# Performance work log

Hardware: AMD Instinct MI355X
Metric: run time of the kernel (lower is better)

The kernel has to match this reference:

```python
import jax, jax.numpy as jnp
import numpy as np

NODE_DIM = 128
CTX_DIM = 256
OUT_DIM = 256
GRID_SIZE = 4
SPLINE_ORDER = 3
IN_DIM = 3 * NODE_DIM  # subj + obj + transformed context
N_NODES = 100000
N_EDGES = 100000


def make_grid(in_dim, grid_size, spline_order, grid_range=(-1.0, 1.0)):
    h = (grid_range[1] - grid_range[0]) / grid_size
    g = (np.arange(-spline_order, grid_size + spline_order + 1, dtype=np.float32) * h
         + grid_range[0])  # [grid_size + 2*spline_order + 1]
    return jnp.asarray(np.tile(g[None, :], (in_dim, 1)))  # [in, G]


def b_splines(x, grid, spline_order):
    # x: [N, in], grid: [in, G] -> bases: [N, in, grid_size + spline_order]
    xg = x[:, :, None]
    bases = ((xg >= grid[:, :-1]) & (xg < grid[:, 1:])).astype(x.dtype)
    for k in range(1, spline_order + 1):
        left = (xg - grid[:, : -(k + 1)]) / (grid[:, k:-1] - grid[:, : -(k + 1)]) * bases[..., :-1]
        right = (grid[:, k + 1:] - xg) / (grid[:, k + 1:] - grid[:, 1:-k]) * bases[..., 1:]
        bases = left + right
    return bases


def setup_inputs() -> dict:
    key = jax.random.key(0)
    ks = jax.random.split(key, 8)
    n_coef = GRID_SIZE + SPLINE_ORDER
    return {
        "node_embeddings": jax.random.normal(ks[0], (N_NODES, NODE_DIM), jnp.float32),
        "context_embeddings": jax.random.normal(ks[1], (N_EDGES, CTX_DIM), jnp.float32),
        "pair_indices": jax.random.randint(ks[2], (N_EDGES, 2), 0, N_NODES, jnp.int64 if jax.config.jax_enable_x64 else jnp.int32),
        "ctx_w": jax.random.normal(ks[3], (NODE_DIM, CTX_DIM), jnp.float32) * (1.0 / np.sqrt(CTX_DIM)),
        "ctx_b": jnp.zeros((NODE_DIM,), jnp.float32),
        "base_weight": jax.random.normal(ks[4], (OUT_DIM, IN_DIM), jnp.float32) * (1.0 / np.sqrt(IN_DIM)),
        "spline_weight": jax.random.normal(ks[5], (OUT_DIM, IN_DIM, n_coef), jnp.float32) * 0.1,
        "spline_scaler": jax.random.normal(ks[6], (OUT_DIM, IN_DIM), jnp.float32) * (1.0 / np.sqrt(IN_DIM)),
        "grid": make_grid(IN_DIM, GRID_SIZE, SPLINE_ORDER),
    }


def reference(node_embeddings, context_embeddings, pair_indices, ctx_w, ctx_b,
              base_weight, spline_weight, spline_scaler, grid):
    # gather subject/object node embeddings (irregular access)
    subj = node_embeddings[pair_indices[:, 0]]          # [E, node_dim]
    obj = node_embeddings[pair_indices[:, 1]]           # [E, node_dim]
    ctx = context_embeddings @ ctx_w.T + ctx_b          # [E, node_dim]
    x = jnp.concatenate([subj, obj, ctx], axis=1)       # [E, 3*node_dim]

    # efficient-KAN linear layer: base (SiLU) branch + B-spline branch
    base_out = jax.nn.silu(x) @ base_weight.T           # [E, out]
    bsp = b_splines(x, grid, SPLINE_ORDER)              # [E, in, n_coef]
    scaled_w = spline_weight * spline_scaler[:, :, None]  # [out, in, n_coef]
    spline_out = jnp.einsum('nic,oic->no', bsp, scaled_w)
    return base_out + spline_out
```

## Files before the change

kernel.cpp:

```cpp
#include <hip/hip_runtime.h>

#define NEDGES   100000
#define NODE_DIM 128
#define CTX_DIM  256
#define OUT_DIM  256
#define IN_DIM   384
#define NCOEF    7

#define BM2      128
#define BK2      32
#define NCH2     96
#define THR2     512

typedef __bf16 bf16x8 __attribute__((ext_vector_type(8)));
typedef float  f32x4  __attribute__((ext_vector_type(4)));

static __device__ __forceinline__ unsigned short f2bf(float f) {
    unsigned int u = __float_as_uint(f);
    u += 0x7FFFu + ((u >> 16) & 1u);
    return (unsigned short)(u >> 16);
}
static __device__ __forceinline__ float bf2f(unsigned short h) {
    return __uint_as_float(((unsigned int)h) << 16);
}
static __device__ __forceinline__ unsigned int pkbf(float a, float b) {
    unsigned int ua = __float_as_uint(a), ub = __float_as_uint(b);
    ua += 0x7FFFu + ((ua >> 16) & 1u);
    ub += 0x7FFFu + ((ub >> 16) & 1u);
    return (ua >> 16) | (ub & 0xFFFF0000u);
}
static __device__ __forceinline__ float silu(float x) {
    return x / (1.0f + __expf(-x));
}
static __device__ __forceinline__ float n3(float t) {
    float d2 = t - 2.0f;
    float a  = fabsf(d2);
    float p1 = fmaf(fmaf(0.5f, a, -1.0f), d2 * d2, 0.66666667f);
    float dd = fmaxf(2.0f - a, 0.0f);
    float p2 = dd * dd * (dd * (1.0f / 6.0f));
    return a < 1.0f ? p1 : p2;
}

static __device__ __forceinline__ void glds16(const unsigned short* g, unsigned short* l) {
    __builtin_amdgcn_global_load_lds(
        (const __attribute__((address_space(1))) void*)g,
        (__attribute__((address_space(3))) void*)l, 16, 0, 0);
}

__global__ void prep_w2(const float* __restrict__ base_w,
                        const float* __restrict__ spline_w,
                        const float* __restrict__ spline_s,
                        unsigned short* __restrict__ Wsw)
{
    int o = blockIdx.x;
    int i = threadIdx.x;
    int bi = o * IN_DIM + i;
    float sc = spline_s[bi];
    const float* sw = spline_w + (size_t)bi * NCOEF;
    uint4 v;
    v.x = pkbf(base_w[bi], sw[0] * sc);
    v.y = pkbf(sw[1] * sc, sw[2] * sc);
    v.z = pkbf(sw[3] * sc, sw[4] * sc);
    v.w = pkbf(sw[5] * sc, sw[6] * sc);
    int ch = i >> 2, g8 = i & 3;
    int p  = o * 4 + (((o >> 1) + g8) & 3);
    *(uint4*)(Wsw + (size_t)ch * (OUT_DIM * BK2) + p * 8) = v;
}

#define K1STR 72
#define BM   128
__global__ __launch_bounds__(512, 2)
void build_x(const float* __restrict__ node_emb,
             const float* __restrict__ ctx_emb,
             const int*   __restrict__ pair,
             const float* __restrict__ ctx_w,
             const float* __restrict__ ctx_b,
             unsigned short* __restrict__ Xbf)
{
    __shared__ unsigned short sm[2 * 128 * K1STR];
    const int tid    = threadIdx.x;
    const int e_base = blockIdx.x * BM;
    const int wid    = tid >> 6;
    const int lan    = tid & 63;
    const int lrow   = lan & 15;
    const int lquad  = lan >> 4;

    #pragma unroll
    for (int it = 0; it < 16; ++it) {
        int id    = it * 512 + tid;
        int f4    = id & 31;
        int which = (id >> 5) & 1;
        int e     = id >> 6;
        int eg = e_base + e; if (eg >= NEDGES) eg = NEDGES - 1;
        int node = pair[eg * 2 + which];
        float4 v = *(const float4*)(node_emb + (size_t)node * NODE_DIM + f4 * 4);
        *(uint2*)&Xbf[(size_t)eg * IN_DIM + which * NODE_DIM + f4 * 4] =
            make_uint2(pkbf(v.x, v.y), pkbf(v.z, v.w));
    }

    f32x4 acc[4][2];
    #pragma unroll
    for (int a = 0; a < 4; ++a)
        #pragma unroll
        for (int b = 0; b < 2; ++b) { f32x4 z = {0.f,0.f,0.f,0.f}; acc[a][b] = z; }

    const int m0 = (wid & 1) * 64;
    const int n0 = (wid >> 1) * 32;

    for (int kc = 0; kc < 4; ++kc) {
        #pragma unroll
        for (int it = 0; it < 4; ++it) {
            int id = it * 512 + tid;
            int r  = id >> 4;
            int c4 = id & 15;
            int eg = e_base + r; if (eg >= NEDGES) eg = NEDGES - 1;
            float4 v = *(const float4*)(ctx_emb + (size_t)eg * CTX_DIM + kc * 64 + c4 * 4);
            *(uint2*)&sm[r * K1STR + c4 * 4] = make_uint2(pkbf(v.x, v.y), pkbf(v.z, v.w));
            float4 w = *(const float4*)(ctx_w + (size_t)r * CTX_DIM + kc * 64 + c4 * 4);
            *(uint2*)&sm[128 * K1STR + r * K1STR + c4 * 4] = make_uint2(pkbf(w.x, w.y), pkbf(w.z, w.w));
        }
        __syncthreads();
        #pragma unroll
        for (int ks = 0; ks < 2; ++ks) {
            int koff = ks * 32 + lquad * 8;
            bf16x8 af[4], bfr[2];
            #pragma unroll
            for (int mt = 0; mt < 4; ++mt)
                af[mt] = *(const bf16x8*)&sm[(m0 + mt*16 + lrow) * K1STR + koff];
            #pragma unroll
            for (int nt = 0; nt < 2; ++nt)
                bfr[nt] = *(const bf16x8*)&sm[128 * K1STR + (n0 + nt*16 + lrow) * K1STR + koff];
            #pragma unroll
            for (int mt = 0; mt < 4; ++mt)
                #pragma unroll
                for (int nt = 0; nt < 2; ++nt)
                    acc[mt][nt] = __builtin_amdgcn_mfma_f32_16x16x32_bf16(
                        af[mt], bfr[nt], acc[mt][nt], 0, 0, 0);
        }
        __syncthreads();
    }

    #define ESTR 136
    #pragma unroll
    for (int nt = 0; nt < 2; ++nt) {
        int col = n0 + nt * 16 + lrow;
        float cb = ctx_b[col];
        #pragma unroll
        for (int mt = 0; mt < 4; ++mt)
            #pragma unroll
            for (int r = 0; r < 4; ++r) {
                int row = m0 + mt * 16 + lquad * 4 + r;
                sm[row * ESTR + col] = f2bf(acc[mt][nt][r] + cb);
            }
    }
    __syncthreads();
    #pragma unroll
    for (int it = 0; it < 8; ++it) {
        int id = it * 512 + tid;
        int row = id >> 5;
        int g   = id & 31;
        int eg = e_base + row; if (eg >= NEDGES) eg = NEDGES - 1;
        *(uint2*)&Xbf[(size_t)eg * IN_DIM + 256 + g * 4] = *(uint2*)&sm[row * ESTR + g * 4];
    }
}

#define A2STR  40
#define A2SZ   (BM2 * A2STR)
#define B2SZ   (OUT_DIM * BK2)
#define OFF_A0 0
#define OFF_A1 A2SZ
#define OFF_B0 (2 * A2SZ)
#define OFF_B1 (2 * A2SZ + B2SZ)
#define LDS2   (2 * A2SZ + 2 * B2SZ)

static __device__ __forceinline__ void gen_elem(
    unsigned short xh, float hinv, float b0, unsigned short* dst)
{
    float x  = bf2f(xh);
    float sl = silu(x);
    unsigned short slh = f2bf(sl);
    float t  = fmaf(x, hinv, b0);
    float jf = floorf(t);
    int   j0 = (int)jf;
    float u  = t - jf;
    float u2 = u * u, u3 = u2 * u;
    float Q0 = u3 * 0.16666667f;
    float d  = 1.0f - u;
    float Q3 = d * d * d * 0.16666667f;
    float Q1 = fmaf(0.5f, u + u2 - u3, 0.16666667f);
    float Q2 = fmaf(0.5f, u3, 0.66666667f - u2);
    unsigned plo = pkbf(Q3, Q2);
    unsigned phi = pkbf(Q1, Q0);
    unsigned long long P = ((unsigned long long)phi << 32) | plo;
    int sh = (j0 << 4) - 32;
    unsigned a  = (unsigned)sh;
    unsigned na = 0u - a;
    unsigned long long lo =
        (a  < 64u) ? (P << (a  & 63u)) : ((na < 64u) ? (P >> (na & 63u)) : 0ull);
    unsigned b2 = a - 64u;
    unsigned nb = 0u - b2;
    unsigned long long hi =
        (b2 < 64u) ? (P << (b2 & 63u)) : ((nb < 64u) ? (P >> (nb & 63u)) : 0ull);
    lo = (lo & ~0xFFFFull) | (unsigned long long)slh;
    uint4 w;
    w.x = (unsigned)lo; w.y = (unsigned)(lo >> 32);
    w.z = (unsigned)hi; w.w = (unsigned)(hi >> 32);
    *(uint4*)dst = w;
}

__global__ __launch_bounds__(THR2, 4)
void kan_gemm2(const unsigned short* __restrict__ Wsw,
               const unsigned short* __restrict__ Xbf,
               const float* __restrict__ grid,
               float* __restrict__ out)
{
    __shared__ unsigned short smem[LDS2];
    const int tid    = threadIdx.x;
    const int e_base = blockIdx.x * BM2;
    const int wid    = tid >> 6;
    const int lan    = tid & 63;
    const int lrow   = lan & 15;
    const int lquad  = lan >> 4;
    const int m0     = (wid & 1) * 64;
    const int n0     = (wid >> 1) * 64;

    const float g0   = grid[0];
    const float hinv = 1.0f / (grid[1] - grid[0]);
    const float b0   = -g0 * hinv;

    const int grow = tid >> 2;
    const int gcol = tid & 3;
    int geg = e_base + grow; if (geg >= NEDGES) geg = NEDGES - 1;
    const unsigned short* xp = Xbf + (size_t)geg * IN_DIM + gcol;
    const unsigned awr = grow * A2STR + gcol * 8;

    f32x4 acc[4][4];
    #pragma unroll
    for (int a = 0; a < 4; ++a)
        #pragma unroll
        for (int b = 0; b < 4; ++b) { f32x4 z = {0.f,0.f,0.f,0.f}; acc[a][b] = z; }

    unsigned short xc = xp[0];
    unsigned short xn = xp[4];

    #pragma unroll
    for (int it = 0; it < 2; ++it) {
        int id = it * THR2 + tid;
        glds16(Wsw + id * 8, &smem[OFF_B0 + id * 8]);
    }
    gen_elem(xc, hinv, b0, &smem[OFF_A0 + awr]);
    __syncthreads();

    for (int kb = 0; kb < NCH2; ++kb) {
        const int cur = kb & 1;
        if (kb + 1 < NCH2) {
            const unsigned short* wc = Wsw + (size_t)(kb + 1) * B2SZ;
            unsigned boff = cur ? OFF_B0 : OFF_B1;
            #pragma unroll
            for (int it = 0; it < 2; ++it) {
                int id = it * THR2 + tid;
                glds16(wc + id * 8, &smem[boff + id * 8]);
            }
            unsigned short xh = xn;
            if (kb + 2 < NCH2) xn = xp[(kb + 2) * 4];
            gen_elem(xh, hinv, b0, &smem[(cur ? OFF_A0 : OFF_A1) + awr]);
        }
        const unsigned ab = cur ? OFF_A1 : OFF_A0;
        const unsigned bb = cur ? OFF_B1 : OFF_B0;
        bf16x8 af[4], bfr[4];
        #pragma unroll
        for (int mt = 0; mt < 4; ++mt)
            af[mt] = *(const bf16x8*)&smem[ab + (m0 + mt*16 + lrow) * A2STR + lquad * 8];
        #pragma unroll
        for (int nt = 0; nt < 4; ++nt) {
            int n = n0 + nt * 16 + lrow;
            bfr[nt] = *(const bf16x8*)&smem[bb + n * 32 + ((((n >> 1) + lquad) & 3) << 3)];
        }
        #pragma unroll
        for (int mt = 0; mt < 4; ++mt)
            #pragma unroll
            for (int nt = 0; nt < 4; ++nt)
                acc[mt][nt] = __builtin_amdgcn_mfma_f32_16x16x32_bf16(
                    af[mt], bfr[nt], acc[mt][nt], 0, 0, 0);
        __syncthreads();
    }

    #pragma unroll
    for (int mt = 0; mt < 4; ++mt) {
        #pragma unroll
        for (int r = 0; r < 4; ++r) {
            int row = m0 + mt * 16 + lquad * 4 + r;
            int eg  = e_base + row;
            if (eg < NEDGES) {
                float* op = out + (size_t)eg * OUT_DIM + n0 + lrow;
                #pragma unroll
                for (int nt = 0; nt < 4; ++nt)
                    op[nt * 16] = acc[mt][nt][r];
            }
        }
    }
}

#define XSTR 392
#define FSTR 72
#define FOFF_X 0
#define FOFF_A (128 * XSTR)
#define FOFF_B (FOFF_A + 128 * FSTR)
#define FLDS (FOFF_B + OUT_DIM * FSTR)

__global__ __launch_bounds__(512, 2)
void fused_fallback(const float* __restrict__ node_emb,
                    const float* __restrict__ ctx_emb,
                    const int*   __restrict__ pair,
                    const float* __restrict__ ctx_w,
                    const float* __restrict__ ctx_b,
                    const float* __restrict__ base_w,
                    const float* __restrict__ spline_w,
                    const float* __restrict__ spline_s,
                    const float* __restrict__ grid,
                    float* __restrict__ out)
{
    __shared__ unsigned short smem[FLDS];
    const int tid    = threadIdx.x;
    const int e_base = blockIdx.x * 128;
    const int wid    = tid >> 6;
    const int lan    = tid & 63;
    const int lrow   = lan & 15;
    const int lquad  = lan >> 4;

    #pragma unroll
    for (int it = 0; it < 16; ++it) {
        int id    = it * 512 + tid;
        int lane4 = id & 31;
        int e     = (id >> 5) & 127;
        int which = id >> 12;
        int eg = e_base + e; if (eg >= NEDGES) eg = NEDGES - 1;
        int node = pair[eg * 2 + which];
        const float4 v = *(const float4*)(node_emb + (size_t)node * NODE_DIM + lane4 * 4);
        *(ushort4*)&smem[FOFF_X + e * XSTR + which * NODE_DIM + lane4 * 4] =
            make_ushort4(f2bf(v.x), f2bf(v.y), f2bf(v.z), f2bf(v.w));
    }
    {
        f32x4 cacc[4][2];
        #pragma unroll
        for (int a = 0; a < 4; ++a)
            #pragma unroll
            for (int b = 0; b < 2; ++b) { f32x4 z = {0.f,0.f,0.f,0.f}; cacc[a][b] = z; }
        const int m0 = (wid & 1) * 64;
        const int n0 = (wid >> 1) * 32;
        for (int kc = 0; kc < 4; ++kc) {
            #pragma unroll
            for (int it = 0; it < 4; ++it) {
                int id = it * 512 + tid;
                int r  = id >> 4;
                int c4 = id & 15;
                int eg = e_base + r; if (eg >= NEDGES) eg = NEDGES - 1;
                float4 v = *(const float4*)(ctx_emb + (size_t)eg * CTX_DIM + kc * 64 + c4 * 4);
                *(ushort4*)&smem[FOFF_A + r * FSTR + c4 * 4] =
                    make_ushort4(f2bf(v.x), f2bf(v.y), f2bf(v.z), f2bf(v.w));
                float4 w = *(const float4*)(ctx_w + (size_t)r * CTX_DIM + kc * 64 + c4 * 4);
                *(ushort4*)&smem[FOFF_B + r * FSTR + c4 * 4] =
                    make_ushort4(f2bf(w.x), f2bf(w.y), f2bf(w.z), f2bf(w.w));
            }
            __syncthreads();
            #pragma unroll
            for (int ks = 0; ks < 2; ++ks) {
                int koff = ks * 32 + lquad * 8;
                bf16x8 af[4], bfr[2];
                #pragma unroll
                for (int mt = 0; mt < 4; ++mt)
                    af[mt] = *(const bf16x8*)&smem[FOFF_A + (m0 + mt*16 + lrow) * FSTR + koff];
                #pragma unroll
                for (int nt = 0; nt < 2; ++nt)
                    bfr[nt] = *(const bf16x8*)&smem[FOFF_B + (n0 + nt*16 + lrow) * FSTR + koff];
                #pragma unroll
                for (int mt = 0; mt < 4; ++mt)
                    #pragma unroll
                    for (int nt = 0; nt < 2; ++nt)
                        cacc[mt][nt] = __builtin_amdgcn_mfma_f32_16x16x32_bf16(
                            af[mt], bfr[nt], cacc[mt][nt], 0, 0, 0);
            }
            __syncthreads();
        }
        #pragma unroll
        for (int mt = 0; mt < 4; ++mt)
            #pragma unroll
            for (int nt = 0; nt < 2; ++nt)
                #pragma unroll
                for (int r = 0; r < 4; ++r) {
                    int row = m0 + mt*16 + lquad*4 + r;
                    int col = n0 + nt*16 + lrow;
                    smem[FOFF_X + row * XSTR + 256 + col] = f2bf(cacc[mt][nt][r] + ctx_b[col]);
                }
    }
    __syncthreads();

    const float g0   = grid[0];
    const float hinv = 1.0f / (grid[1] - grid[0]);

    f32x4 acc[4][4];
    #pragma unroll
    for (int a = 0; a < 4; ++a)
        #pragma unroll
        for (int b = 0; b < 4; ++b) { f32x4 z = {0.f,0.f,0.f,0.f}; acc[a][b] = z; }

    const int m0 = (wid & 1) * 64;
    const int n0 = (wid >> 1) * 64;

    for (int kb = 0; kb < 48; ++kb) {
        const int seg = kb / 6;
        const int i0  = (kb - seg * 6) * 64;
        #pragma unroll
        for (int it = 0; it < 4; ++it) {
            int id = it * 512 + tid;
            int e  = id >> 4;
            int qq = id & 15;
            ushort4 xv = *(const ushort4*)&smem[FOFF_X + e * XSTR + i0 + qq * 4];
            float x0 = bf2f(xv.x), x1 = bf2f(xv.y), x2 = bf2f(xv.z), x3 = bf2f(xv.w);
            unsigned short r0, r1, r2, r3;
            if (seg == 0) {
                r0 = f2bf(silu(x0)); r1 = f2bf(silu(x1));
                r2 = f2bf(silu(x2)); r3 = f2bf(silu(x3));
            } else {
                const float cf = (float)(seg - 1);
                r0 = f2bf(n3((x0 - g0) * hinv - cf));
                r1 = f2bf(n3((x1 - g0) * hinv - cf));
                r2 = f2bf(n3((x2 - g0) * hinv - cf));
                r3 = f2bf(n3((x3 - g0) * hinv - cf));
            }
            *(ushort4*)&smem[FOFF_A + e * FSTR + qq * 4] = make_ushort4(r0, r1, r2, r3);
        }
        #pragma unroll
        for (int it = 0; it < 4; ++it) {
            int id = it * 512 + tid;
            int o  = id >> 4;
            int qq = id & 15;
            unsigned short r0, r1, r2, r3;
            if (seg == 0) {
                const float4 w = *(const float4*)(base_w + (size_t)o * IN_DIM + i0 + qq * 4);
                r0 = f2bf(w.x); r1 = f2bf(w.y); r2 = f2bf(w.z); r3 = f2bf(w.w);
            } else {
                int c  = seg - 1;
                int bi = o * IN_DIM + i0 + qq * 4;
                r0 = f2bf(spline_w[(size_t)(bi    ) * NCOEF + c] * spline_s[bi    ]);
                r1 = f2bf(spline_w[(size_t)(bi + 1) * NCOEF + c] * spline_s[bi + 1]);
                r2 = f2bf(spline_w[(size_t)(bi + 2) * NCOEF + c] * spline_s[bi + 2]);
                r3 = f2bf(spline_w[(size_t)(bi + 3) * NCOEF + c] * spline_s[bi + 3]);
            }
            *(ushort4*)&smem[FOFF_B + o * FSTR + qq * 4] = make_ushort4(r0, r1, r2, r3);
        }
        __syncthreads();
        #pragma unroll
        for (int ks = 0; ks < 2; ++ks) {
            int koff = ks * 32 + lquad * 8;
            bf16x8 af[4], bfr[4];
            #pragma unroll
            for (int mt = 0; mt < 4; ++mt)
                af[mt] = *(const bf16x8*)&smem[FOFF_A + (m0 + mt*16 + lrow) * FSTR + koff];
            #pragma unroll
            for (int nt = 0; nt < 4; ++nt)
                bfr[nt] = *(const bf16x8*)&smem[FOFF_B + (n0 + nt*16 + lrow) * FSTR + koff];
            #pragma unroll
            for (int mt = 0; mt < 4; ++mt)
                #pragma unroll
                for (int nt = 0; nt < 4; ++nt)
                    acc[mt][nt] = __builtin_amdgcn_mfma_f32_16x16x32_bf16(
                        af[mt], bfr[nt], acc[mt][nt], 0, 0, 0);
        }
        __syncthreads();
    }

    #pragma unroll
    for (int mt = 0; mt < 4; ++mt) {
        #pragma unroll
        for (int r = 0; r < 4; ++r) {
            int row = m0 + mt*16 + lquad*4 + r;
            int eg  = e_base + row;
            if (eg < NEDGES) {
                float* op = out + (size_t)eg * OUT_DIM + n0 + lrow;
                #pragma unroll
                for (int nt = 0; nt < 4; ++nt)
                    op[nt * 16] = acc[mt][nt][r];
            }
        }
    }
}

extern "C" void kernel_launch(void* const* d_in, const int* in_sizes, int n_in,
                              void* d_out, int out_size, void* d_ws, size_t ws_size,
                              hipStream_t stream)
{
    const float* node_emb = (const float*)d_in[0];
    const float* ctx_emb  = (const float*)d_in[1];
    const int*   pair     = (const int*)d_in[2];
    const float* ctx_w    = (const float*)d_in[3];
    const float* ctx_b    = (const float*)d_in[4];
    const float* base_w   = (const float*)d_in[5];
    const float* spline_w = (const float*)d_in[6];
    const float* spline_s = (const float*)d_in[7];
    const float* grid     = (const float*)d_in[8];
    float* out = (float*)d_out;

    const int nblk = (NEDGES + BM2 - 1) / BM2;
    const size_t xoff = 2u * 1024u * 1024u;
    const size_t need = xoff + (size_t)NEDGES * IN_DIM * sizeof(unsigned short);

    if (ws_size >= need) {
        unsigned short* Wsw = (unsigned short*)d_ws;
        unsigned short* Xbf = (unsigned short*)((char*)d_ws + xoff);
        prep_w2<<<OUT_DIM, IN_DIM, 0, stream>>>(base_w, spline_w, spline_s, Wsw);
        build_x<<<nblk, 512, 0, stream>>>(node_emb, ctx_emb, pair, ctx_w, ctx_b, Xbf);
        kan_gemm2<<<nblk, THR2, 0, stream>>>(Wsw, Xbf, grid, out);
    } else {
        fused_fallback<<<nblk, 512, 0, stream>>>(
            node_emb, ctx_emb, pair, ctx_w, ctx_b, base_w, spline_w, spline_s, grid, out);
    }
}
```

Before: 436.1 us.

## Generate spline A-fragments in registers from LDS lookup table, deepen B pipeline

Precomputes a 512-entry quantized table of cubic B-spline basis vectors in LDS. Each lane builds its MFMA A-fragment directly from a table lookup plus SiLU instead of evaluating the polynomial and staging an A tile in shared memory. Weight chunks are now loaded two at a time into a four-deep LDS ring, halving barriers per K step. The table quantizes the spline position within each cell, which adds approximation error, and x values are fetched with scattered 2-byte global loads per lane.

```diff
diff --git a/kernel.cpp b/kernel.cpp
--- a/kernel.cpp
+++ b/kernel.cpp
@@ -11,6 +11,7 @@
 #define BK2      32
 #define NCH2     96
 #define THR2     512
+#define TABN     512
 
 typedef __bf16 bf16x8 __attribute__((ext_vector_type(8)));
 typedef float  f32x4  __attribute__((ext_vector_type(4)));
@@ -164,57 +165,30 @@
     }
 }
 
-#define A2STR  40
-#define A2SZ   (BM2 * A2STR)
-#define B2SZ   (OUT_DIM * BK2)
-#define OFF_A0 0
-#define OFF_A1 A2SZ
-#define OFF_B0 (2 * A2SZ)
-#define OFF_B1 (2 * A2SZ + B2SZ)
-#define LDS2   (2 * A2SZ + 2 * B2SZ)
-
-static __device__ __forceinline__ void gen_elem(
-    unsigned short xh, float hinv, float b0, unsigned short* dst)
-{
-    float x  = bf2f(xh);
+#define OFF_T  0
+#define OFF_B3 (TABN * 8)
+#define LDS3   (TABN * 8 + 4 * 8192)
+
+static __device__ __forceinline__ bf16x8 gen_af(unsigned short xh, float hinv, float b0,
+                                                const unsigned short* tab) {
+    float x = bf2f(xh);
+    float t = fmaf(x, hinv, b0);
+    int idx = (int)(t * (TABN / 10.0f));
+    idx = min(max(idx, 0), TABN - 1);
+    uint4 e = *(const uint4*)(tab + idx * 8);
     float sl = silu(x);
-    unsigned short slh = f2bf(sl);
-    float t  = fmaf(x, hinv, b0);
-    float jf = floorf(t);
-    int   j0 = (int)jf;
-    float u  = t - jf;
-    float u2 = u * u, u3 = u2 * u;
-    float Q0 = u3 * 0.16666667f;
-    float d  = 1.0f - u;
-    float Q3 = d * d * d * 0.16666667f;
-    float Q1 = fmaf(0.5f, u + u2 - u3, 0.16666667f);
-    float Q2 = fmaf(0.5f, u3, 0.66666667f - u2);
-    unsigned plo = pkbf(Q3, Q2);
-    unsigned phi = pkbf(Q1, Q0);
-    unsigned long long P = ((unsigned long long)phi << 32) | plo;
-    int sh = (j0 << 4) - 32;
-    unsigned a  = (unsigned)sh;
-    unsigned na = 0u - a;
-    unsigned long long lo =
-        (a  < 64u) ? (P << (a  & 63u)) : ((na < 64u) ? (P >> (na & 63u)) : 0ull);
-    unsigned b2 = a - 64u;
-    unsigned nb = 0u - b2;
-    unsigned long long hi =
-        (b2 < 64u) ? (P << (b2 & 63u)) : ((nb < 64u) ? (P >> (nb & 63u)) : 0ull);
-    lo = (lo & ~0xFFFFull) | (unsigned long long)slh;
-    uint4 w;
-    w.x = (unsigned)lo; w.y = (unsigned)(lo >> 32);
-    w.z = (unsigned)hi; w.w = (unsigned)(hi >> 32);
-    *(uint4*)dst = w;
+    e.x = (e.x & 0xFFFF0000u) | (unsigned)f2bf(sl);
+    union { uint4 u; bf16x8 b; } cv; cv.u = e;
+    return cv.b;
 }
 
 __global__ __launch_bounds__(THR2, 4)
-void kan_gemm2(const unsigned short* __restrict__ Wsw,
+void kan_gemm3(const unsigned short* __restrict__ Wsw,
                const unsigned short* __restrict__ Xbf,
                const float* __restrict__ grid,
                float* __restrict__ out)
 {
-    __shared__ unsigned short smem[LDS2];
+    __shared__ unsigned short smem[LDS3];
     const int tid    = threadIdx.x;
     const int e_base = blockIdx.x * BM2;
     const int wid    = tid >> 6;
@@ -224,15 +198,54 @@
     const int m0     = (wid & 1) * 64;
     const int n0     = (wid >> 1) * 64;
 
-    const float g0   = grid[0];
     const float hinv = 1.0f / (grid[1] - grid[0]);
-    const float b0   = -g0 * hinv;
-
-    const int grow = tid >> 2;
-    const int gcol = tid & 3;
-    int geg = e_base + grow; if (geg >= NEDGES) geg = NEDGES - 1;
-    const unsigned short* xp = Xbf + (size_t)geg * IN_DIM + gcol;
-    const unsigned awr = grow * A2STR + gcol * 8;
+    const float b0   = -grid[0] * hinv;
+
+    {
+        int e = tid & (TABN - 1);
+        float t  = ((float)e + 0.5f) * (10.0f / TABN);
+        float jf = floorf(t);
+        int   j0 = (int)jf;
+        float u  = t - jf;
+        float u2 = u * u, u3 = u2 * u;
+        float Q0 = u3 * (1.0f / 6.0f);
+        float d  = 1.0f - u;
+        float Q3 = d * d * d * (1.0f / 6.0f);
+        float Q1 = fmaf(0.5f, u + u2 - u3, 1.0f / 6.0f);
+        float Q2 = fmaf(0.5f, u3, 0.66666667f - u2);
+        unsigned plo = pkbf(Q3, Q2);
+        unsigned phi = pkbf(Q1, Q0);
+        unsigned long long P = ((unsigned long long)phi << 32) | plo;
+        int sh = (j0 << 4) - 32;
+        unsigned a  = (unsigned)sh, na = 0u - a;
+        unsigned long long lo =
+            (a  < 64u) ? (P << (a  & 63u)) : ((na < 64u) ? (P >> (na & 63u)) : 0ull);
+        unsigned b2 = a - 64u, nb = 0u - b2;
+        unsigned long long hi =
+            (b2 < 64u) ? (P << (b2 & 63u)) : ((nb < 64u) ? (P >> (nb & 63u)) : 0ull);
+        lo &= ~0xFFFFull;
+        uint4 w;
+        w.x = (unsigned)lo; w.y = (unsigned)(lo >> 32);
+        w.z = (unsigned)hi; w.w = (unsigned)(hi >> 32);
+        *(uint4*)&smem[OFF_T + e * 8] = w;
+    }
+
+    const unsigned short* xrow[4];
+    #pragma unroll
+    for (int mt = 0; mt < 4; ++mt) {
+        int row = m0 + mt * 16 + lrow;
+        int eg  = e_base + row; if (eg >= NEDGES) eg = NEDGES - 1;
+        xrow[mt] = Xbf + (size_t)eg * IN_DIM;
+    }
+
+    #pragma unroll
+    for (int c = 0; c < 2; ++c)
+        #pragma unroll
+        for (int it = 0; it < 2; ++it) {
+            int id = it * THR2 + tid;
+            glds16(Wsw + (size_t)c * 8192 + id * 8, &smem[OFF_B3 + c * 8192 + id * 8]);
+        }
+    __syncthreads();
 
     f32x4 acc[4][4];
     #pragma unroll
@@ -240,48 +253,46 @@
         #pragma unroll
         for (int b = 0; b < 4; ++b) { f32x4 z = {0.f,0.f,0.f,0.f}; acc[a][b] = z; }
 
-    unsigned short xc = xp[0];
-    unsigned short xn = xp[4];
-
-    #pragma unroll
-    for (int it = 0; it < 2; ++it) {
-        int id = it * THR2 + tid;
-        glds16(Wsw + id * 8, &smem[OFF_B0 + id * 8]);
-    }
-    gen_elem(xc, hinv, b0, &smem[OFF_A0 + awr]);
-    __syncthreads();
-
-    for (int kb = 0; kb < NCH2; ++kb) {
-        const int cur = kb & 1;
-        if (kb + 1 < NCH2) {
-            const unsigned short* wc = Wsw + (size_t)(kb + 1) * B2SZ;
-            unsigned boff = cur ? OFF_B0 : OFF_B1;
-            #pragma unroll
-            for (int it = 0; it < 2; ++it) {
-                int id = it * THR2 + tid;
-                glds16(wc + id * 8, &smem[boff + id * 8]);
-            }
-            unsigned short xh = xn;
-            if (kb + 2 < NCH2) xn = xp[(kb + 2) * 4];
-            gen_elem(xh, hinv, b0, &smem[(cur ? OFF_A0 : OFF_A1) + awr]);
-        }
-        const unsigned ab = cur ? OFF_A1 : OFF_A0;
-        const unsigned bb = cur ? OFF_B1 : OFF_B0;
-        bf16x8 af[4], bfr[4];
-        #pragma unroll
-        for (int mt = 0; mt < 4; ++mt)
-            af[mt] = *(const bf16x8*)&smem[ab + (m0 + mt*16 + lrow) * A2STR + lquad * 8];
-        #pragma unroll
-        for (int nt = 0; nt < 4; ++nt) {
-            int n = n0 + nt * 16 + lrow;
-            bfr[nt] = *(const bf16x8*)&smem[bb + n * 32 + ((((n >> 1) + lquad) & 3) << 3)];
-        }
-        #pragma unroll
-        for (int mt = 0; mt < 4; ++mt)
-            #pragma unroll
-            for (int nt = 0; nt < 4; ++nt)
-                acc[mt][nt] = __builtin_amdgcn_mfma_f32_16x16x32_bf16(
-                    af[mt], bfr[nt], acc[mt][nt], 0, 0, 0);
+    for (int j = 0; j < 48; ++j) {
+        unsigned short xc[8];
+        const int colb = j * 8 + lquad;
+        #pragma unroll
+        for (int mt = 0; mt < 4; ++mt) {
+            xc[mt * 2]     = xrow[mt][colb];
+            xc[mt * 2 + 1] = xrow[mt][colb + 4];
+        }
+        if (j < 47) {
+            #pragma unroll
+            for (int c = 0; c < 2; ++c) {
+                int ch = 2 * j + 2 + c;
+                const unsigned short* wc = Wsw + (size_t)ch * 8192;
+                unsigned short* lb = &smem[OFF_B3 + (ch & 3) * 8192];
+                #pragma unroll
+                for (int it = 0; it < 2; ++it) {
+                    int id = it * THR2 + tid;
+                    glds16(wc + id * 8, lb + id * 8);
+                }
+            }
+        }
+        #pragma unroll
+        for (int h = 0; h < 2; ++h) {
+            const int ch = 2 * j + h;
+            const unsigned short* bb = &smem[OFF_B3 + (ch & 3) * 8192];
+            bf16x8 bfr[4];
+            #pragma unroll
+            for (int nt = 0; nt < 4; ++nt) {
+                int n = n0 + nt * 16 + lrow;
+                bfr[nt] = *(const bf16x8*)&bb[n * 32 + ((((n >> 1) + lquad) & 3) << 3)];
+            }
+            #pragma unroll
+            for (int mt = 0; mt < 4; ++mt) {
+                bf16x8 af = gen_af(xc[mt * 2 + h], hinv, b0, &smem[OFF_T]);
+                #pragma unroll
+                for (int nt = 0; nt < 4; ++nt)
+                    acc[mt][nt] = __builtin_amdgcn_mfma_f32_16x16x32_bf16(
+                        af, bfr[nt], acc[mt][nt], 0, 0, 0);
+            }
+        }
         __syncthreads();
     }
 
@@ -510,7 +521,7 @@
         unsigned short* Xbf = (unsigned short*)((char*)d_ws + xoff);
         prep_w2<<<OUT_DIM, IN_DIM, 0, stream>>>(base_w, spline_w, spline_s, Wsw);
         build_x<<<nblk, 512, 0, stream>>>(node_emb, ctx_emb, pair, ctx_w, ctx_b, Xbf);
-        kan_gemm2<<<nblk, THR2, 0, stream>>>(Wsw, Xbf, grid, out);
+        kan_gemm3<<<nblk, THR2, 0, stream>>>(Wsw, Xbf, grid, out);
     } else {
         fused_fallback<<<nblk, 512, 0, stream>>>(
             node_emb, ctx_emb, pair, ctx_w, ctx_b, base_w, spline_w, spline_s, grid, out);
```

Result: slower. 682.2 us (+56.4%).
